# Optimization experiments

Hardware: AMD Instinct MI355X
Metric: run time of the kernel (lower is better)

Reference implementation:

```python
import jax, jax.numpy as jnp
import numpy as np

B, C, H, W = 8, 256, 64, 64
C8 = C // 8


def setup_inputs() -> dict:
    key = jax.random.key(0)
    ks = jax.random.split(key, 8)
    x = jax.random.normal(ks[0], (B, C, H, W), dtype=jnp.float32)
    # 1x1 convs == channel matmuls; store as [out_ch, in_ch] plus bias
    Wq = jax.random.normal(ks[1], (C8, C), dtype=jnp.float32) * (1.0 / np.sqrt(C))
    bq = jnp.zeros((C8,), dtype=jnp.float32)
    Wk = jax.random.normal(ks[2], (C8, C), dtype=jnp.float32) * (1.0 / np.sqrt(C))
    bk = jnp.zeros((C8,), dtype=jnp.float32)
    Wv = jax.random.normal(ks[3], (C, C), dtype=jnp.float32) * (1.0 / np.sqrt(C))
    bv = jnp.zeros((C,), dtype=jnp.float32)
    # gamma initialized to zero in the module, but use a nonzero value so the
    # attention branch actually contributes to the output being checked
    gamma = jnp.full((1,), 0.5, dtype=jnp.float32)
    return {"x": x, "Wq": Wq, "bq": bq, "Wk": Wk, "bk": bk, "Wv": Wv, "bv": bv, "gamma": gamma}


def reference(x, Wq, bq, Wk, bk, Wv, bv, gamma):
    b, c, h, w = x.shape
    n = h * w
    xf = x.reshape(b, c, n)                                  # [B, C, N]
    q = jnp.einsum('oc,bcn->bon', Wq, xf) + bq[None, :, None]  # [B, C8, N]
    k = jnp.einsum('oc,bcn->bon', Wk, xf) + bk[None, :, None]  # [B, C8, N]
    v = jnp.einsum('oc,bcn->bon', Wv, xf) + bv[None, :, None]  # [B, C,  N]
    # attention[b, i, j] = sum_d q[b, d, i] * k[b, d, j]  (no 1/sqrt(d) scaling!)
    scores = jnp.einsum('bdi,bdj->bij', q, k)                # [B, N, N]
    attn = jax.nn.softmax(scores, axis=-1)                   # softmax over j
    # out[b, c, i] = sum_j v[b, c, j] * attn[b, i, j]
    out = jnp.einsum('bcj,bij->bci', v, attn)                # [B, C, N]
    out = out.reshape(b, c, h, w)
    return gamma[0] * out + x
```

## Files before the change

kernel.cpp:

```cpp
#include <hip/hip_runtime.h>
#include <math.h>

#define BB 8
#define CC 256
#define NN 4096

typedef float f4 __attribute__((ext_vector_type(4)));
typedef short bh8 __attribute__((ext_vector_type(8)));

__device__ __forceinline__ unsigned short f2bf(float f) {
    unsigned u = __builtin_bit_cast(unsigned, f);
    u += 0x7fff + ((u >> 16) & 1);
    return (unsigned short)(u >> 16);
}

__device__ __forceinline__ float exp2_fast(float x) {
    float r;
    asm("v_exp_f32 %0, %1" : "=v"(r) : "v"(x));
    return r;
}

__global__ void prep_w_kernel(const float* __restrict__ Wq, const float* __restrict__ bq,
                              const float* __restrict__ Wk, const float* __restrict__ bk,
                              const float* __restrict__ Wv, const float* __restrict__ bv,
                              float* __restrict__ WcatT, float* __restrict__ bcat) {
    const float L2E = 1.4426950408889634f;
    int idx = blockIdx.x * 256 + threadIdx.x;
    if (idx < 320) {
        bcat[idx] = (idx < 32) ? bq[idx] * L2E : (idx < 64 ? bk[idx - 32] : bv[idx - 64]);
    }
    if (idx < 320 * 256) {
        int o = idx >> 8;
        int c = idx & 255;
        float v = (o < 32) ? Wq[o * 256 + c] * L2E
                           : (o < 64 ? Wk[(o - 32) * 256 + c] : Wv[(o - 64) * 256 + c]);
        WcatT[c * 320 + o] = v;
    }
}

__global__ __launch_bounds__(256, 2) void qkv_kernel(
    const float* __restrict__ x, const float* __restrict__ WcatT,
    const float* __restrict__ bcat,
    unsigned short* __restrict__ q64, unsigned short* __restrict__ k64,
    unsigned short* __restrict__ vC) {
    __shared__ float xs[256 * 64];
    __shared__ unsigned short qkl[64 * 128];
    unsigned short* vsl = (unsigned short*)xs;

    int blk = blockIdx.x;
    int b = blk >> 6;
    int i0 = (blk & 63) << 6;
    int t = threadIdx.x;

    const float* xb = x + ((size_t)b << 20);
    for (int idx = t; idx < 256 * 64; idx += 256) {
        int c = idx >> 6, ii = idx & 63;
        xs[idx] = xb[((size_t)c << 12) + i0 + ii];
    }
    __syncthreads();

    int to = t & 63;
    int tp = t >> 6;

    float acc[80];
#pragma unroll
    for (int uo = 0; uo < 5; ++uo) {
        float bias = bcat[to + 64 * uo];
#pragma unroll
        for (int pi = 0; pi < 16; ++pi) acc[uo * 16 + pi] = bias;
    }

    for (int c = 0; c < 256; ++c) {
        const float* wc = WcatT + c * 320 + to;
        float w0 = wc[0];
        float w1 = wc[64];
        float w2 = wc[128];
        float w3 = wc[192];
        float w4 = wc[256];
        const float4* xr = (const float4*)(xs + c * 64 + 16 * tp);
#pragma unroll
        for (int q = 0; q < 4; ++q) {
            float4 xv = xr[q];
#pragma unroll
            for (int e = 0; e < 4; ++e) {
                int pi = 4 * q + e;
                float xe = (e == 0) ? xv.x : (e == 1) ? xv.y : (e == 2) ? xv.z : xv.w;
                acc[0 * 16 + pi] += w0 * xe;
                acc[1 * 16 + pi] += w1 * xe;
                acc[2 * 16 + pi] += w2 * xe;
                acc[3 * 16 + pi] += w3 * xe;
                acc[4 * 16 + pi] += w4 * xe;
            }
        }
    }
    __syncthreads();

#pragma unroll
    for (int pi = 0; pi < 16; ++pi) {
        int ii = 16 * tp + pi;
        float v = acc[pi];
        unsigned short hi = f2bf(v);
        float vhi = __builtin_bit_cast(float, ((unsigned)hi) << 16);
        unsigned short lo = f2bf(v - vhi);
        if (to < 32) {
            qkl[ii * 128 + to] = hi;
            qkl[ii * 128 + 32 + to] = lo;
        } else {
            qkl[ii * 128 + 32 + to] = hi;
            qkl[ii * 128 + 64 + to] = lo;
        }
    }
#pragma unroll
    for (int uo = 1; uo < 5; ++uo) {
#pragma unroll
        for (int pi = 0; pi < 16; ++pi) {
            int c = to + 64 * (uo - 1);
            int ii = 16 * tp + pi;
            vsl[c * 66 + ii] = f2bf(acc[uo * 16 + pi]);
        }
    }
    __syncthreads();

    const unsigned* qk32 = (const unsigned*)qkl;
    unsigned* qb = (unsigned*)(q64 + ((size_t)(b * NN + i0)) * 64);
    unsigned* kb = (unsigned*)(k64 + ((size_t)(b * NN + i0)) * 64);
    for (int idx = t; idx < 64 * 32; idx += 256) {
        int row = idx >> 5, dw = idx & 31;
        qb[row * 32 + dw] = qk32[row * 64 + dw];
        kb[row * 32 + dw] = qk32[row * 64 + 32 + dw];
    }
    for (int idx = t; idx < 256 * 32; idx += 256) {
        int c = idx >> 5, dw = idx & 31;
        unsigned val = *(const unsigned*)(vsl + c * 66 + 2 * dw);
        *(unsigned*)(vC + ((size_t)(b * CC + c)) * NN + i0 + 2 * dw) = val;
    }
}

__global__ __launch_bounds__(256, 2) void attn_kernel(
    const unsigned short* __restrict__ q64, const unsigned short* __restrict__ k64,
    const unsigned short* __restrict__ vC, const float* __restrict__ x,
    const float* __restrict__ gamma, float* __restrict__ out) {
    __shared__ unsigned short vs[2][256 * 64];

    int t = threadIdx.x;
    int lane = t & 63;
    int w = t >> 6;
    int g = lane >> 4;
    int li = lane & 15;
    int blk = blockIdx.x;
    int b = blk & 7;
    int i0 = (blk >> 3) << 6;
    int qb = i0 + 16 * w;

    const unsigned short* vb = vC + ((size_t)b * CC) * NN;
    const unsigned short* kb = k64 + ((size_t)b * NN) * 64;

    bh8 qf[2];
#pragma unroll
    for (int s = 0; s < 2; ++s)
        qf[s] = *(const bh8*)(q64 + ((size_t)(b * NN + qb + li)) * 64 + s * 32 + 8 * g);

    const unsigned short* vsrcb[8];
#pragma unroll
    for (int s = 0; s < 8; ++s) {
        int c = 64 * w + 8 * s + (lane >> 3);
        int slot = (lane & 7) ^ (c & 7);
        vsrcb[s] = vb + (size_t)c * NN + slot * 8;
    }
    const unsigned short* ksrcb[8];
#pragma unroll
    for (int jt = 0; jt < 4; ++jt)
#pragma unroll
        for (int s = 0; s < 2; ++s)
            ksrcb[jt * 2 + s] = kb + (size_t)(16 * jt + li) * 64 + s * 32 + 8 * g;

    f4 acc[16];
#pragma unroll
    for (int ct = 0; ct < 16; ++ct) acc[ct] = (f4){0.f, 0.f, 0.f, 0.f};
    float m = -INFINITY, l = 0.f;

    auto stageV = [&](int buf, int j0) {
#pragma unroll
        for (int s = 0; s < 8; ++s) {
            __builtin_amdgcn_global_load_lds(
                (const __attribute__((address_space(1))) unsigned int*)(vsrcb[s] + j0),
                (__attribute__((address_space(3))) unsigned int*)(&vs[buf][(64 * w + 8 * s) * 64]),
                16, 0, 0);
        }
    };
    auto loadK = [&](bh8 (&kf)[4][2], int j0) {
        size_t joff = (size_t)j0 * 64;
#pragma unroll
        for (int jt = 0; jt < 4; ++jt)
#pragma unroll
            for (int s = 0; s < 2; ++s)
                kf[jt][s] = *(const bh8*)(ksrcb[jt * 2 + s] + joff);
    };
    auto qkComp = [&](f4 (&sOut)[4], bh8 (&kc)[4][2]) {
#pragma unroll
        for (int jt = 0; jt < 4; ++jt) {
            f4 a = {0.f, 0.f, 0.f, 0.f};
            a = __builtin_amdgcn_mfma_f32_16x16x32_bf16(kc[jt][0], qf[0], a, 0, 0, 0);
            a = __builtin_amdgcn_mfma_f32_16x16x32_bf16(kc[jt][1], qf[0], a, 0, 0, 0);
            a = __builtin_amdgcn_mfma_f32_16x16x32_bf16(kc[jt][0], qf[1], a, 0, 0, 0);
            sOut[jt] = a;
        }
    };
    auto mkpb = [&](f4 (&sCur)[4], int h) -> bh8 {
        unsigned pk[2][2];
#pragma unroll
        for (int tl = 0; tl < 2; ++tl)
#pragma unroll
            for (int pp = 0; pp < 2; ++pp) {
                unsigned lo16 = f2bf(sCur[2 * h + tl][2 * pp]);
                unsigned hi16 = f2bf(sCur[2 * h + tl][2 * pp + 1]);
                pk[tl][pp] = lo16 | (hi16 << 16);
            }
        union { unsigned u[4]; bh8 v; } un;
#pragma unroll
        for (int d = 0; d < 4; ++d) {
            int srcl = (((2 * g + (d >> 1)) & 3) << 4) | li;
            unsigned a0 = (unsigned)__shfl((int)pk[0][d & 1], srcl);
            unsigned a1 = (unsigned)__shfl((int)pk[1][d & 1], srcl);
            un.u[d] = (g >> 1) ? a1 : a0;
        }
        return un.v;
    };

    bh8 kf0[4][2], kf1[4][2];
    f4 sA[4], sB[4];

    stageV(0, 0);
    loadK(kf0, 0);
    loadK(kf1, 64);
    qkComp(sA, kf0);
    __syncthreads();

    auto step = [&](int tt, bh8 (&kNext)[4][2], bh8 (&kLoad)[4][2],
                    f4 (&sCur)[4], f4 (&sNxt)[4], int buf) {
        if (tt < 63) stageV(buf ^ 1, (tt + 1) << 6);
        if (tt < 62) loadK(kLoad, (tt + 2) << 6);

        if (tt < 63) qkComp(sNxt, kNext);

        float mx = sCur[0][0];
#pragma unroll
        for (int jt = 0; jt < 4; ++jt)
#pragma unroll
            for (int e = 0; e < 4; ++e) mx = fmaxf(mx, sCur[jt][e]);
        mx = fmaxf(mx, __shfl_xor(mx, 16));
        mx = fmaxf(mx, __shfl_xor(mx, 32));
        if (!__all(mx <= m + 11.541561f)) {
            float mnew = fmaxf(m, mx);
            float sc = exp2_fast(m - mnew);
            l *= sc;
#pragma unroll
            for (int ct = 0; ct < 16; ++ct)
#pragma unroll
                for (int e = 0; e < 4; ++e) acc[ct][e] *= sc;
            m = mnew;
        }
        float sum = 0.f;
#pragma unroll
        for (int jt = 0; jt < 4; ++jt)
#pragma unroll
            for (int e = 0; e < 4; ++e) {
                float p = exp2_fast(sCur[jt][e] - m);
                sCur[jt][e] = p;
                sum += p;
            }
        sum += __shfl_xor(sum, 16);
        sum += __shfl_xor(sum, 32);
        l += sum;

        const char* vsb = (const char*)vs[buf];
#pragma unroll
        for (int h = 0; h < 2; ++h) {
            bh8 pb = mkpb(sCur, h);
            __builtin_amdgcn_s_setprio(1);
#pragma unroll
            for (int ct = 0; ct < 16; ++ct) {
                int c = 16 * ct + li;
                int off = c * 128 + ((64 * h + 16 * g) ^ ((c & 7) << 4));
                bh8 vf = *(const bh8*)(vsb + off);
                acc[ct] = __builtin_amdgcn_mfma_f32_16x16x32_bf16(vf, pb, acc[ct], 0, 0, 0);
            }
            __builtin_amdgcn_s_setprio(0);
        }
        __syncthreads();
    };

    for (int tt = 0; tt < 64; tt += 2) {
        step(tt, kf1, kf0, sA, sB, 0);
        step(tt + 1, kf0, kf1, sB, sA, 1);
    }

    float gm = gamma[0];
    float rl = 1.f / l;
    const float* xb = x + ((size_t)b * CC) * NN;
    float* ob = out + ((size_t)b * CC) * NN;
    int i = qb + li;
#pragma unroll
    for (int ct = 0; ct < 16; ++ct)
#pragma unroll
        for (int e = 0; e < 4; ++e) {
            int c = 16 * ct + 4 * g + e;
            size_t idx = (size_t)c * NN + i;
            ob[idx] = gm * (acc[ct][e] * rl) + xb[idx];
        }
}

extern "C" void kernel_launch(void* const* d_in, const int* in_sizes, int n_in,
                              void* d_out, int out_size, void* d_ws, size_t ws_size,
                              hipStream_t stream) {
    const float* x = (const float*)d_in[0];
    const float* Wq = (const float*)d_in[1];
    const float* bq = (const float*)d_in[2];
    const float* Wk = (const float*)d_in[3];
    const float* bk = (const float*)d_in[4];
    const float* Wv = (const float*)d_in[5];
    const float* bv = (const float*)d_in[6];
    const float* gamma = (const float*)d_in[7];
    float* out = (float*)d_out;

    unsigned short* ws16 = (unsigned short*)d_ws;
    unsigned short* q64w = ws16;
    unsigned short* k64w = ws16 + 2097152;
    unsigned short* vCw = ws16 + 4194304;
    float* WcatT = (float*)((char*)d_ws + 25165824);
    float* bcat = WcatT + 81920;

    prep_w_kernel<<<320, 256, 0, stream>>>(Wq, bq, Wk, bk, Wv, bv, WcatT, bcat);
    qkv_kernel<<<BB * (NN / 64), 256, 0, stream>>>(x, WcatT, bcat, q64w, k64w, vCw);
    attn_kernel<<<512, 256, 0, stream>>>(q64w, k64w, vCw, x, gamma, out);
}
```

Measured before the change: 232.0 us.

## Process two query tiles per wave to reuse K and V fragments

```diff
diff --git a/kernel.cpp b/kernel.cpp
--- a/kernel.cpp
+++ b/kernel.cpp
@@ -136,7 +136,7 @@
     }
 }
 
-__global__ __launch_bounds__(256, 2) void attn_kernel(
+__global__ __launch_bounds__(256, 1) void attn_kernel(
     const unsigned short* __restrict__ q64, const unsigned short* __restrict__ k64,
     const unsigned short* __restrict__ vC, const float* __restrict__ x,
     const float* __restrict__ gamma, float* __restrict__ out) {
@@ -149,16 +149,19 @@
     int li = lane & 15;
     int blk = blockIdx.x;
     int b = blk & 7;
-    int i0 = (blk >> 3) << 6;
-    int qb = i0 + 16 * w;
+    int i0 = (blk >> 3) << 7;
+    int qbA = i0 + 32 * w;
+    int qbB = i0 + 32 * w + 16;
 
     const unsigned short* vb = vC + ((size_t)b * CC) * NN;
     const unsigned short* kb = k64 + ((size_t)b * NN) * 64;
 
-    bh8 qf[2];
-#pragma unroll
-    for (int s = 0; s < 2; ++s)
-        qf[s] = *(const bh8*)(q64 + ((size_t)(b * NN + qb + li)) * 64 + s * 32 + 8 * g);
+    bh8 qfA[2], qfB[2];
+#pragma unroll
+    for (int s = 0; s < 2; ++s) {
+        qfA[s] = *(const bh8*)(q64 + ((size_t)(b * NN + qbA + li)) * 64 + s * 32 + 8 * g);
+        qfB[s] = *(const bh8*)(q64 + ((size_t)(b * NN + qbB + li)) * 64 + s * 32 + 8 * g);
+    }
 
     const unsigned short* vsrcb[8];
 #pragma unroll
@@ -174,10 +177,13 @@
         for (int s = 0; s < 2; ++s)
             ksrcb[jt * 2 + s] = kb + (size_t)(16 * jt + li) * 64 + s * 32 + 8 * g;
 
-    f4 acc[16];
-#pragma unroll
-    for (int ct = 0; ct < 16; ++ct) acc[ct] = (f4){0.f, 0.f, 0.f, 0.f};
-    float m = -INFINITY, l = 0.f;
+    f4 accA[16], accB[16];
+#pragma unroll
+    for (int ct = 0; ct < 16; ++ct) {
+        accA[ct] = (f4){0.f, 0.f, 0.f, 0.f};
+        accB[ct] = (f4){0.f, 0.f, 0.f, 0.f};
+    }
+    float mA = -INFINITY, lA = 0.f, mB = -INFINITY, lB = 0.f;
 
     auto stageV = [&](int buf, int j0) {
 #pragma unroll
@@ -196,53 +202,17 @@
             for (int s = 0; s < 2; ++s)
                 kf[jt][s] = *(const bh8*)(ksrcb[jt * 2 + s] + joff);
     };
-    auto qkComp = [&](f4 (&sOut)[4], bh8 (&kc)[4][2]) {
+    auto qkComp = [&](f4 (&sOut)[4], bh8 (&kc)[4][2], bh8 (&qq)[2]) {
 #pragma unroll
         for (int jt = 0; jt < 4; ++jt) {
             f4 a = {0.f, 0.f, 0.f, 0.f};
-            a = __builtin_amdgcn_mfma_f32_16x16x32_bf16(kc[jt][0], qf[0], a, 0, 0, 0);
-            a = __builtin_amdgcn_mfma_f32_16x16x32_bf16(kc[jt][1], qf[0], a, 0, 0, 0);
-            a = __builtin_amdgcn_mfma_f32_16x16x32_bf16(kc[jt][0], qf[1], a, 0, 0, 0);
+            a = __builtin_amdgcn_mfma_f32_16x16x32_bf16(kc[jt][0], qq[0], a, 0, 0, 0);
+            a = __builtin_amdgcn_mfma_f32_16x16x32_bf16(kc[jt][1], qq[0], a, 0, 0, 0);
+            a = __builtin_amdgcn_mfma_f32_16x16x32_bf16(kc[jt][0], qq[1], a, 0, 0, 0);
             sOut[jt] = a;
         }
     };
-    auto mkpb = [&](f4 (&sCur)[4], int h) -> bh8 {
-        unsigned pk[2][2];
-#pragma unroll
-        for (int tl = 0; tl < 2; ++tl)
-#pragma unroll
-            for (int pp = 0; pp < 2; ++pp) {
-                unsigned lo16 = f2bf(sCur[2 * h + tl][2 * pp]);
-                unsigned hi16 = f2bf(sCur[2 * h + tl][2 * pp + 1]);
-                pk[tl][pp] = lo16 | (hi16 << 16);
-            }
-        union { unsigned u[4]; bh8 v; } un;
-#pragma unroll
-        for (int d = 0; d < 4; ++d) {
-            int srcl = (((2 * g + (d >> 1)) & 3) << 4) | li;
-            unsigned a0 = (unsigned)__shfl((int)pk[0][d & 1], srcl);
-            unsigned a1 = (unsigned)__shfl((int)pk[1][d & 1], srcl);
-            un.u[d] = (g >> 1) ? a1 : a0;
-        }
-        return un.v;
-    };
-
-    bh8 kf0[4][2], kf1[4][2];
-    f4 sA[4], sB[4];
-
-    stageV(0, 0);
-    loadK(kf0, 0);
-    loadK(kf1, 64);
-    qkComp(sA, kf0);
-    __syncthreads();
-
-    auto step = [&](int tt, bh8 (&kNext)[4][2], bh8 (&kLoad)[4][2],
-                    f4 (&sCur)[4], f4 (&sNxt)[4], int buf) {
-        if (tt < 63) stageV(buf ^ 1, (tt + 1) << 6);
-        if (tt < 62) loadK(kLoad, (tt + 2) << 6);
-
-        if (tt < 63) qkComp(sNxt, kNext);
-
+    auto softmax = [&](f4 (&sCur)[4], f4 (&acc)[16], float& m, float& l) {
         float mx = sCur[0][0];
 #pragma unroll
         for (int jt = 0; jt < 4; ++jt)
@@ -272,18 +242,64 @@
         sum += __shfl_xor(sum, 16);
         sum += __shfl_xor(sum, 32);
         l += sum;
+    };
+    auto mkpb = [&](f4 (&sCur)[4], int h) -> bh8 {
+        unsigned pk[2][2];
+#pragma unroll
+        for (int tl = 0; tl < 2; ++tl)
+#pragma unroll
+            for (int pp = 0; pp < 2; ++pp) {
+                unsigned lo16 = f2bf(sCur[2 * h + tl][2 * pp]);
+                unsigned hi16 = f2bf(sCur[2 * h + tl][2 * pp + 1]);
+                pk[tl][pp] = lo16 | (hi16 << 16);
+            }
+        union { unsigned u[4]; bh8 v; } un;
+#pragma unroll
+        for (int d = 0; d < 4; ++d) {
+            int srcl = (((2 * g + (d >> 1)) & 3) << 4) | li;
+            unsigned a0 = (unsigned)__shfl((int)pk[0][d & 1], srcl);
+            unsigned a1 = (unsigned)__shfl((int)pk[1][d & 1], srcl);
+            un.u[d] = (g >> 1) ? a1 : a0;
+        }
+        return un.v;
+    };
+
+    bh8 kf0[4][2], kf1[4][2];
+    f4 sA0[4], sB0[4], sA1[4], sB1[4];
+
+    stageV(0, 0);
+    loadK(kf0, 0);
+    loadK(kf1, 64);
+    qkComp(sA0, kf0, qfA);
+    qkComp(sB0, kf0, qfB);
+    __syncthreads();
+
+    auto step = [&](int tt, bh8 (&kNext)[4][2], bh8 (&kLoad)[4][2],
+                    f4 (&sAc)[4], f4 (&sBc)[4], f4 (&sAn)[4], f4 (&sBn)[4], int buf) {
+        if (tt < 63) stageV(buf ^ 1, (tt + 1) << 6);
+        if (tt < 62) loadK(kLoad, (tt + 2) << 6);
+
+        if (tt < 63) {
+            qkComp(sAn, kNext, qfA);
+            qkComp(sBn, kNext, qfB);
+        }
+
+        softmax(sAc, accA, mA, lA);
+        softmax(sBc, accB, mB, lB);
 
         const char* vsb = (const char*)vs[buf];
 #pragma unroll
         for (int h = 0; h < 2; ++h) {
-            bh8 pb = mkpb(sCur, h);
+            bh8 pba = mkpb(sAc, h);
+            bh8 pbb = mkpb(sBc, h);
             __builtin_amdgcn_s_setprio(1);
 #pragma unroll
             for (int ct = 0; ct < 16; ++ct) {
                 int c = 16 * ct + li;
                 int off = c * 128 + ((64 * h + 16 * g) ^ ((c & 7) << 4));
                 bh8 vf = *(const bh8*)(vsb + off);
-                acc[ct] = __builtin_amdgcn_mfma_f32_16x16x32_bf16(vf, pb, acc[ct], 0, 0, 0);
+                accA[ct] = __builtin_amdgcn_mfma_f32_16x16x32_bf16(vf, pba, accA[ct], 0, 0, 0);
+                accB[ct] = __builtin_amdgcn_mfma_f32_16x16x32_bf16(vf, pbb, accB[ct], 0, 0, 0);
             }
             __builtin_amdgcn_s_setprio(0);
         }
@@ -291,22 +307,26 @@
     };
 
     for (int tt = 0; tt < 64; tt += 2) {
-        step(tt, kf1, kf0, sA, sB, 0);
-        step(tt + 1, kf0, kf1, sB, sA, 1);
+        step(tt, kf1, kf0, sA0, sB0, sA1, sB1, 0);
+        step(tt + 1, kf0, kf1, sA1, sB1, sA0, sB0, 1);
     }
 
     float gm = gamma[0];
-    float rl = 1.f / l;
+    float rlA = 1.f / lA;
+    float rlB = 1.f / lB;
     const float* xb = x + ((size_t)b * CC) * NN;
     float* ob = out + ((size_t)b * CC) * NN;
-    int i = qb + li;
+    int iA = qbA + li;
+    int iB = qbB + li;
 #pragma unroll
     for (int ct = 0; ct < 16; ++ct)
 #pragma unroll
         for (int e = 0; e < 4; ++e) {
             int c = 16 * ct + 4 * g + e;
-            size_t idx = (size_t)c * NN + i;
-            ob[idx] = gm * (acc[ct][e] * rl) + xb[idx];
+            size_t ia = (size_t)c * NN + iA;
+            size_t ib = (size_t)c * NN + iB;
+            ob[ia] = gm * (accA[ct][e] * rlA) + xb[ia];
+            ob[ib] = gm * (accB[ct][e] * rlB) + xb[ib];
         }
 }
 
@@ -332,5 +352,5 @@
 
     prep_w_kernel<<<320, 256, 0, stream>>>(Wq, bq, Wk, bk, Wv, bv, WcatT, bcat);
     qkv_kernel<<<BB * (NN / 64), 256, 0, stream>>>(x, WcatT, bcat, q64w, k64w, vCw);
-    attn_kernel<<<512, 256, 0, stream>>>(q64w, k64w, vCw, x, gamma, out);
-}
+    attn_kernel<<<256, 256, 0, stream>>>(q64w, k64w, vCw, x, gamma, out);
+}
```

After: 256.3 us. 1.1x slower.

## Halve attention tile to 32 queries and 32-key steps with 128-thread blocks

Applied to the files above, without the earlier changes.

```diff
diff --git a/kernel.cpp b/kernel.cpp
--- a/kernel.cpp
+++ b/kernel.cpp
@@ -136,11 +136,11 @@
     }
 }
 
-__global__ __launch_bounds__(256, 2) void attn_kernel(
+__global__ __launch_bounds__(128, 2) void attn_kernel(
     const unsigned short* __restrict__ q64, const unsigned short* __restrict__ k64,
     const unsigned short* __restrict__ vC, const float* __restrict__ x,
     const float* __restrict__ gamma, float* __restrict__ out) {
-    __shared__ unsigned short vs[2][256 * 64];
+    __shared__ unsigned short vs[2][256 * 32];
 
     int t = threadIdx.x;
     int lane = t & 63;
@@ -149,7 +149,7 @@
     int li = lane & 15;
     int blk = blockIdx.x;
     int b = blk & 7;
-    int i0 = (blk >> 3) << 6;
+    int i0 = (blk >> 3) << 5;
     int qb = i0 + 16 * w;
 
     const unsigned short* vb = vC + ((size_t)b * CC) * NN;
@@ -161,15 +161,19 @@
         qf[s] = *(const bh8*)(q64 + ((size_t)(b * NN + qb + li)) * 64 + s * 32 + 8 * g);
 
     const unsigned short* vsrcb[8];
-#pragma unroll
-    for (int s = 0; s < 8; ++s) {
-        int c = 64 * w + 8 * s + (lane >> 3);
-        int slot = (lane & 7) ^ (c & 7);
-        vsrcb[s] = vb + (size_t)c * NN + slot * 8;
-    }
-    const unsigned short* ksrcb[8];
-#pragma unroll
-    for (int jt = 0; jt < 4; ++jt)
+    {
+        int q4 = lane >> 2;
+        int key = (q4 & 3) ^ ((q4 >> 2) & 3);
+        int piece = (lane & 3) ^ key;
+#pragma unroll
+        for (int s = 0; s < 8; ++s) {
+            int c = 128 * w + 16 * s + q4;
+            vsrcb[s] = vb + (size_t)c * NN + piece * 8;
+        }
+    }
+    const unsigned short* ksrcb[4];
+#pragma unroll
+    for (int jt = 0; jt < 2; ++jt)
 #pragma unroll
         for (int s = 0; s < 2; ++s)
             ksrcb[jt * 2 + s] = kb + (size_t)(16 * jt + li) * 64 + s * 32 + 8 * g;
@@ -184,21 +188,21 @@
         for (int s = 0; s < 8; ++s) {
             __builtin_amdgcn_global_load_lds(
                 (const __attribute__((address_space(1))) unsigned int*)(vsrcb[s] + j0),
-                (__attribute__((address_space(3))) unsigned int*)(&vs[buf][(64 * w + 8 * s) * 64]),
+                (__attribute__((address_space(3))) unsigned int*)(&vs[buf][(128 * w + 16 * s) * 32]),
                 16, 0, 0);
         }
     };
-    auto loadK = [&](bh8 (&kf)[4][2], int j0) {
+    auto loadK = [&](bh8 (&kf)[2][2], int j0) {
         size_t joff = (size_t)j0 * 64;
 #pragma unroll
-        for (int jt = 0; jt < 4; ++jt)
+        for (int jt = 0; jt < 2; ++jt)
 #pragma unroll
             for (int s = 0; s < 2; ++s)
                 kf[jt][s] = *(const bh8*)(ksrcb[jt * 2 + s] + joff);
     };
-    auto qkComp = [&](f4 (&sOut)[4], bh8 (&kc)[4][2]) {
-#pragma unroll
-        for (int jt = 0; jt < 4; ++jt) {
+    auto qkComp = [&](f4 (&sOut)[2], bh8 (&kc)[2][2]) {
+#pragma unroll
+        for (int jt = 0; jt < 2; ++jt) {
             f4 a = {0.f, 0.f, 0.f, 0.f};
             a = __builtin_amdgcn_mfma_f32_16x16x32_bf16(kc[jt][0], qf[0], a, 0, 0, 0);
             a = __builtin_amdgcn_mfma_f32_16x16x32_bf16(kc[jt][1], qf[0], a, 0, 0, 0);
@@ -206,14 +210,14 @@
             sOut[jt] = a;
         }
     };
-    auto mkpb = [&](f4 (&sCur)[4], int h) -> bh8 {
+    auto mkpb = [&](f4 (&sCur)[2]) -> bh8 {
         unsigned pk[2][2];
 #pragma unroll
         for (int tl = 0; tl < 2; ++tl)
 #pragma unroll
             for (int pp = 0; pp < 2; ++pp) {
-                unsigned lo16 = f2bf(sCur[2 * h + tl][2 * pp]);
-                unsigned hi16 = f2bf(sCur[2 * h + tl][2 * pp + 1]);
+                unsigned lo16 = f2bf(sCur[tl][2 * pp]);
+                unsigned hi16 = f2bf(sCur[tl][2 * pp + 1]);
                 pk[tl][pp] = lo16 | (hi16 << 16);
             }
         union { unsigned u[4]; bh8 v; } un;
@@ -227,27 +231,26 @@
         return un.v;
     };
 
-    bh8 kf0[4][2], kf1[4][2];
-    f4 sA[4], sB[4];
+    bh8 kf0[2][2], kf1[2][2];
+    f4 sA[2], sB[2];
 
     stageV(0, 0);
     loadK(kf0, 0);
-    loadK(kf1, 64);
+    loadK(kf1, 32);
     qkComp(sA, kf0);
     __syncthreads();
 
-    auto step = [&](int tt, bh8 (&kNext)[4][2], bh8 (&kLoad)[4][2],
-                    f4 (&sCur)[4], f4 (&sNxt)[4], int buf) {
-        if (tt < 63) stageV(buf ^ 1, (tt + 1) << 6);
-        if (tt < 62) loadK(kLoad, (tt + 2) << 6);
-
-        if (tt < 63) qkComp(sNxt, kNext);
-
-        float mx = sCur[0][0];
-#pragma unroll
-        for (int jt = 0; jt < 4; ++jt)
-#pragma unroll
-            for (int e = 0; e < 4; ++e) mx = fmaxf(mx, sCur[jt][e]);
+    int vbase = 64 * li + 16 * (g ^ ((li & 3) ^ ((li >> 2) & 3)));
+
+    auto step = [&](int tt, bh8 (&kNext)[2][2], bh8 (&kLoad)[2][2],
+                    f4 (&sCur)[2], f4 (&sNxt)[2], int buf) {
+        if (tt < 127) stageV(buf ^ 1, (tt + 1) << 5);
+        if (tt < 126) loadK(kLoad, (tt + 2) << 5);
+
+        if (tt < 127) qkComp(sNxt, kNext);
+
+        float mx = fmaxf(fmaxf(fmaxf(sCur[0][0], sCur[0][1]), fmaxf(sCur[0][2], sCur[0][3])),
+                         fmaxf(fmaxf(sCur[1][0], sCur[1][1]), fmaxf(sCur[1][2], sCur[1][3])));
         mx = fmaxf(mx, __shfl_xor(mx, 16));
         mx = fmaxf(mx, __shfl_xor(mx, 32));
         if (!__all(mx <= m + 11.541561f)) {
@@ -262,7 +265,7 @@
         }
         float sum = 0.f;
 #pragma unroll
-        for (int jt = 0; jt < 4; ++jt)
+        for (int jt = 0; jt < 2; ++jt)
 #pragma unroll
             for (int e = 0; e < 4; ++e) {
                 float p = exp2_fast(sCur[jt][e] - m);
@@ -273,24 +276,19 @@
         sum += __shfl_xor(sum, 32);
         l += sum;
 
+        bh8 pb = mkpb(sCur);
         const char* vsb = (const char*)vs[buf];
-#pragma unroll
-        for (int h = 0; h < 2; ++h) {
-            bh8 pb = mkpb(sCur, h);
-            __builtin_amdgcn_s_setprio(1);
-#pragma unroll
-            for (int ct = 0; ct < 16; ++ct) {
-                int c = 16 * ct + li;
-                int off = c * 128 + ((64 * h + 16 * g) ^ ((c & 7) << 4));
-                bh8 vf = *(const bh8*)(vsb + off);
-                acc[ct] = __builtin_amdgcn_mfma_f32_16x16x32_bf16(vf, pb, acc[ct], 0, 0, 0);
-            }
-            __builtin_amdgcn_s_setprio(0);
-        }
+        __builtin_amdgcn_s_setprio(1);
+#pragma unroll
+        for (int ct = 0; ct < 16; ++ct) {
+            bh8 vf = *(const bh8*)(vsb + ct * 1024 + vbase);
+            acc[ct] = __builtin_amdgcn_mfma_f32_16x16x32_bf16(vf, pb, acc[ct], 0, 0, 0);
+        }
+        __builtin_amdgcn_s_setprio(0);
         __syncthreads();
     };
 
-    for (int tt = 0; tt < 64; tt += 2) {
+    for (int tt = 0; tt < 128; tt += 2) {
         step(tt, kf1, kf0, sA, sB, 0);
         step(tt + 1, kf0, kf1, sB, sA, 1);
     }
@@ -332,5 +330,5 @@
 
     prep_w_kernel<<<320, 256, 0, stream>>>(Wq, bq, Wk, bk, Wv, bv, WcatT, bcat);
     qkv_kernel<<<BB * (NN / 64), 256, 0, stream>>>(x, WcatT, bcat, q64w, k64w, vCw);
-    attn_kernel<<<512, 256, 0, stream>>>(q64w, k64w, vCw, x, gamma, out);
-}
+    attn_kernel<<<1024, 128, 0, stream>>>(q64w, k64w, vCw, x, gamma, out);
+}
```

After: 279.9 us. 20.7% more time.

## Permute V columns to match MFMA P layout, eliminating lane shuffles

Applied to the files above, without the earlier changes.

```diff
diff --git a/kernel.cpp b/kernel.cpp
--- a/kernel.cpp
+++ b/kernel.cpp
@@ -12,6 +12,9 @@
     unsigned u = __builtin_bit_cast(unsigned, f);
     u += 0x7fff + ((u >> 16) & 1);
     return (unsigned short)(u >> 16);
+}
+__device__ __forceinline__ unsigned packbf(float a, float b) {
+    return (unsigned)f2bf(a) | ((unsigned)f2bf(b) << 16);
 }
 
 __device__ __forceinline__ float exp2_fast(float x) {
@@ -132,7 +135,9 @@
     for (int idx = t; idx < 256 * 32; idx += 256) {
         int c = idx >> 5, dw = idx & 31;
         unsigned val = *(const unsigned*)(vsl + c * 66 + 2 * dw);
-        *(unsigned*)(vC + ((size_t)(b * CC + c)) * NN + i0 + 2 * dw) = val;
+        int i = 2 * dw;
+        int p = 32 * (i >> 5) + 8 * ((i >> 2) & 3) + 4 * ((i >> 4) & 1) + (i & 3);
+        *(unsigned*)(vC + ((size_t)(b * CC + c)) * NN + i0 + p) = val;
     }
 }
 
@@ -206,26 +211,6 @@
             sOut[jt] = a;
         }
     };
-    auto mkpb = [&](f4 (&sCur)[4], int h) -> bh8 {
-        unsigned pk[2][2];
-#pragma unroll
-        for (int tl = 0; tl < 2; ++tl)
-#pragma unroll
-            for (int pp = 0; pp < 2; ++pp) {
-                unsigned lo16 = f2bf(sCur[2 * h + tl][2 * pp]);
-                unsigned hi16 = f2bf(sCur[2 * h + tl][2 * pp + 1]);
-                pk[tl][pp] = lo16 | (hi16 << 16);
-            }
-        union { unsigned u[4]; bh8 v; } un;
-#pragma unroll
-        for (int d = 0; d < 4; ++d) {
-            int srcl = (((2 * g + (d >> 1)) & 3) << 4) | li;
-            unsigned a0 = (unsigned)__shfl((int)pk[0][d & 1], srcl);
-            unsigned a1 = (unsigned)__shfl((int)pk[1][d & 1], srcl);
-            un.u[d] = (g >> 1) ? a1 : a0;
-        }
-        return un.v;
-    };
 
     bh8 kf0[4][2], kf1[4][2];
     f4 sA[4], sB[4];
@@ -248,9 +233,9 @@
         for (int jt = 0; jt < 4; ++jt)
 #pragma unroll
             for (int e = 0; e < 4; ++e) mx = fmaxf(mx, sCur[jt][e]);
-        mx = fmaxf(mx, __shfl_xor(mx, 16));
-        mx = fmaxf(mx, __shfl_xor(mx, 32));
         if (!__all(mx <= m + 11.541561f)) {
+            mx = fmaxf(mx, __shfl_xor(mx, 16));
+            mx = fmaxf(mx, __shfl_xor(mx, 32));
             float mnew = fmaxf(m, mx);
             float sc = exp2_fast(m - mnew);
             l *= sc;
@@ -269,14 +254,17 @@
                 sCur[jt][e] = p;
                 sum += p;
             }
-        sum += __shfl_xor(sum, 16);
-        sum += __shfl_xor(sum, 32);
         l += sum;
 
         const char* vsb = (const char*)vs[buf];
 #pragma unroll
         for (int h = 0; h < 2; ++h) {
-            bh8 pb = mkpb(sCur, h);
+            union { unsigned u[4]; bh8 v; } pf;
+            pf.u[0] = packbf(sCur[2 * h + 0][0], sCur[2 * h + 0][1]);
+            pf.u[1] = packbf(sCur[2 * h + 0][2], sCur[2 * h + 0][3]);
+            pf.u[2] = packbf(sCur[2 * h + 1][0], sCur[2 * h + 1][1]);
+            pf.u[3] = packbf(sCur[2 * h + 1][2], sCur[2 * h + 1][3]);
+            bh8 pb = pf.v;
             __builtin_amdgcn_s_setprio(1);
 #pragma unroll
             for (int ct = 0; ct < 16; ++ct) {
@@ -294,6 +282,9 @@
         step(tt, kf1, kf0, sA, sB, 0);
         step(tt + 1, kf0, kf1, sB, sA, 1);
     }
+
+    l += __shfl_xor(l, 16);
+    l += __shfl_xor(l, 32);
 
     float gm = gamma[0];
     float rl = 1.f / l;
```

Result: no change. 235.9 us (+1.7%).
